# Kernel tuning notes

Hardware: AMD Instinct MI355X
Metric: run time of the kernel (lower is better)

## Reference

```python
import jax, jax.numpy as jnp
import numpy as np
from jax import lax

B, DZ, H, U, T, V = 256, 512, 512, 16, 16, 512  # batch, latent, lstm hidden, segments, steps/segment, vocab


def setup_inputs() -> dict:
    key = jax.random.key(0)
    ks = jax.random.split(key, 32)
    w = lambda k, shape: jax.random.normal(k, shape, jnp.float32) * 0.05
    d = {
        'z': jax.random.normal(ks[0], (B, DZ), jnp.float32),
        'x': jax.random.randint(ks[1], (B, U * T), 0, V),
        # conductor init-state projection: DZ -> 4H
        'Wc': w(ks[2], (4 * H, DZ)), 'bc': jnp.zeros((4 * H,), jnp.float32),
        # conductor 2-layer LSTM (input H, hidden H)
        'cWih0': w(ks[3], (4 * H, H)), 'cWhh0': w(ks[4], (4 * H, H)),
        'cbih0': jnp.zeros((4 * H,), jnp.float32), 'cbhh0': jnp.zeros((4 * H,), jnp.float32),
        'cWih1': w(ks[5], (4 * H, H)), 'cWhh1': w(ks[6], (4 * H, H)),
        'cbih1': jnp.zeros((4 * H,), jnp.float32), 'cbhh1': jnp.zeros((4 * H,), jnp.float32),
        # decoder init-state projection: H -> 4H
        'Wd': w(ks[7], (4 * H, H)), 'bd': jnp.zeros((4 * H,), jnp.float32),
        # decoder 2-layer LSTM (layer0 input 2H, layer1 input H, hidden H)
        'dWih0': w(ks[8], (4 * H, 2 * H)), 'dWhh0': w(ks[9], (4 * H, H)),
        'dbih0': jnp.zeros((4 * H,), jnp.float32), 'dbhh0': jnp.zeros((4 * H,), jnp.float32),
        'dWih1': w(ks[10], (4 * H, H)), 'dWhh1': w(ks[11], (4 * H, H)),
        'dbih1': jnp.zeros((4 * H,), jnp.float32), 'dbhh1': jnp.zeros((4 * H,), jnp.float32),
        # token embedding and output distribution head
        'emb': w(ks[12], (V, H)),
        'Wo': w(ks[13], (V, H)), 'bo': jnp.zeros((V,), jnp.float32),
    }
    return d


def _cell(x, h, c, Wih, Whh, bih, bhh):
    # PyTorch LSTM gate order: i, f, g, o
    g = x @ Wih.T + bih + h @ Whh.T + bhh
    i, f, gg, o = jnp.split(g, 4, axis=-1)
    c = jax.nn.sigmoid(f) * c + jax.nn.sigmoid(i) * jnp.tanh(gg)
    h = jax.nn.sigmoid(o) * jnp.tanh(c)
    return h, c


def _lstm_layer(xp, h0, c0, Whh, bhh):
    # xp: [N, T, 4H] = precomputed x @ Wih.T + bih
    def step(carry, xg):
        h, c = carry
        g = xg + h @ Whh.T + bhh
        i, f, gg, o = jnp.split(g, 4, axis=-1)
        c = jax.nn.sigmoid(f) * c + jax.nn.sigmoid(i) * jnp.tanh(gg)
        h = jax.nn.sigmoid(o) * jnp.tanh(c)
        return (h, c), h
    _, ys = lax.scan(step, (h0, c0), jnp.swapaxes(xp, 0, 1))
    return jnp.swapaxes(ys, 0, 1)  # [N, T, H]


def reference(z, x, Wc, bc, cWih0, cWhh0, cbih0, cbhh0, cWih1, cWhh1, cbih1, cbhh1,
              Wd, bd, dWih0, dWhh0, dbih0, dbhh0, dWih1, dWhh1, dbih1, dbhh1,
              emb, Wo, bo):
    Bz = z.shape[0]
    # --- conductor ---
    ci = jnp.tanh(z @ Wc.T + bc)  # [B, 4H]
    h1, h2, c1, c2 = ci[:, :H], ci[:, H:2 * H], ci[:, 2 * H:3 * H], ci[:, 3 * H:]
    o0 = jnp.zeros((Bz, H), ci.dtype)

    def cstep(carry, _):
        o, h1, c1, h2, c2 = carry
        h1, c1 = _cell(o, h1, c1, cWih0, cWhh0, cbih0, cbhh0)
        h2, c2 = _cell(h1, h2, c2, cWih1, cWhh1, cbih1, cbhh1)
        return (h2, h1, c1, h2, c2), h2

    _, couts = lax.scan(cstep, (o0, h1, c1, h2, c2), None, length=U)
    cond_out = jnp.swapaxes(couts, 0, 1)  # [B, U, H]

    # --- decoder init states ---
    states = jnp.tanh(cond_out @ Wd.T + bd).reshape(Bz * U, 4 * H)
    dh1, dh2, dc1, dc2 = (states[:, :H], states[:, H:2 * H],
                          states[:, 2 * H:3 * H], states[:, 3 * H:])
    h_init = dh1 + dh2  # [BU, H]

    # --- teacher-forced decoder ---
    xt = x.reshape(Bz * U, T)
    e = emb[xt]  # [BU, T, H]
    e = jnp.concatenate([jnp.zeros((Bz * U, 1, H), e.dtype), e[:, :-1]], axis=1)
    inp = jnp.concatenate(
        [e, jnp.broadcast_to(h_init[:, None], (Bz * U, T, H))], axis=-1)  # [BU, T, 2H]

    y0 = _lstm_layer(inp @ dWih0.T + dbih0, dh1, dc1, dWhh0, dbhh0)
    y1 = _lstm_layer(y0 @ dWih1.T + dbih1, dh2, dc2, dWhh1, dbhh1)
    dist = jax.nn.softmax(y1 @ Wo.T + bo, axis=-1)  # [BU, T, V]
    return dist.reshape(Bz, U * T, V)
```

## Files before the change

### kernel.cpp

```cpp
#include <hip/hip_runtime.h>
#include <math.h>

#define AS1 __attribute__((address_space(1)))
#define AS3 __attribute__((address_space(3)))

typedef __attribute__((ext_vector_type(8))) short short8v;
typedef __attribute__((ext_vector_type(16))) float f32x16;

constexpr size_t PA4c = (size_t)4096 * 512;
constexpr size_t PABc = (size_t)256 * 512;

__device__ __forceinline__ float sigmoidf_(float x) { return 1.f / (1.f + expf(-x)); }
__device__ __forceinline__ unsigned int f2bfu(float f) {
    unsigned int u = __float_as_uint(f);
    return (u + 0x7FFF + ((u >> 16) & 1)) >> 16;
}
__device__ __forceinline__ float bf2f(unsigned int s) { return __uint_as_float(s << 16); }
__device__ __forceinline__ unsigned int pack2(float v) {
    unsigned int b0 = f2bfu(v);
    unsigned int b1 = f2bfu(v - bf2f(b0));
    return b0 | (b1 << 16);
}
__device__ __forceinline__ float unpack2(unsigned int p) { return bf2f(p & 0xffffu) + bf2f(p >> 16); }

__device__ __forceinline__ void xswz(int d, int ngx, int ngy, int& bx, int& by) {
    int nwg = ngx * ngy;
    int q = nwg >> 3, r = nwg & 7, xcd = d & 7, pos = d >> 3;
    int logical = (xcd < r ? xcd * (q + 1) : r * (q + 1) + (xcd - r) * q) + pos;
    bx = logical % ngx; by = logical / ngx;
}

__device__ __forceinline__ void xswz_col(int d, int ngx, int ngy, int& bx, int& by) {
    int cpx = ngx >> 3;
    int xcd = d & 7, j = d >> 3;
    bx = xcd * cpx + (j % cpx);
    by = j / cpx;
}

__device__ __forceinline__ size_t offf(int m, int k) {
    return ((size_t)((m >> 5) * 64 + (k >> 3))) * 256 + (size_t)((m & 31) * 8 + (k & 7));
}

template<int N>
__device__ __forceinline__ void wait_vm() {
    asm volatile("s_waitcnt vmcnt(%0) lgkmcnt(0)" :: "n"(N) : "memory");
}

template<int FM, int FN>
__device__ __forceinline__ void gemm_core(
    const short* __restrict__ A1, const short* __restrict__ B1,
    const short* __restrict__ A2, const short* __restrict__ B2,
    int M, int N, int nsteps, int pairSwitch,
    int bx, int by, short* lds, f32x16 (&acc)[FM][FN])
{
    constexpr int ABLK = 4 * FM, BBLK = 2 * FN;
    constexpr int ACH = 2 * ABLK * 2, BCH = 2 * BBLK * 2;
    constexpr int CHT = ACH + BCH;
    constexpr int CPW = CHT / 8;
    constexpr int NBUF = 3;
    constexpr int BUFSH = CHT * 512;
    const int tid = threadIdx.x, lane = tid & 63, wid = tid >> 6;
    const int wm = wid >> 1, wn = wid & 1;
    const int l31 = lane & 31, loct = lane >> 5;
    const int mblk0 = by * ABLK, nblk0 = bx * BBLK;
    const size_t planeA = (size_t)M * 512, planeB = (size_t)N * 512;

    const short* cur[CPW];
    const short* nxt[CPW];
    int ldo[CPW];
    #pragma unroll
    for (int i = 0; i < CPW; ++i) {
        int c = wid * CPW + i;
        ldo[i] = c * 512;
        size_t off;
        const short *b1, *b2;
        if (c < ACH) {
            int plane = c / (ABLK * 2), rem = c % (ABLK * 2), blk = rem >> 1, piece = rem & 1;
            off = (size_t)plane * planeA + (size_t)(mblk0 + blk) * 16384 + piece * 512 + lane * 8;
            b1 = A1; b2 = A2;
        } else {
            int cb = c - ACH;
            int plane = cb / (BBLK * 2), rem = cb % (BBLK * 2), blk = rem >> 1, piece = rem & 1;
            off = (size_t)plane * planeB + (size_t)(nblk0 + blk) * 16384 + piece * 512 + lane * 8;
            b1 = B1; b2 = B2;
        }
        cur[i] = b1 + off;
        nxt[i] = b2 ? (b2 + off) : (b1 + off);
    }

    #pragma unroll
    for (int fm = 0; fm < FM; ++fm)
        #pragma unroll
        for (int fn = 0; fn < FN; ++fn)
            acc[fm][fn] = (f32x16){};

    auto STAGE = [&](int bufIdx) {
        short* db = lds + bufIdx * BUFSH;
        #pragma unroll
        for (int i = 0; i < CPW; ++i) {
            __builtin_amdgcn_global_load_lds((const AS1 unsigned int*)cur[i],
                                             (AS3 unsigned int*)(db + ldo[i]), 16, 0, 0);
            cur[i] += 1024;
        }
    };

    STAGE(0); STAGE(1);
    wait_vm<CPW>();
    __builtin_amdgcn_s_barrier();

    for (int t = 0; t < nsteps; ++t) {
        int s = t + NBUF - 1;
        if (s < nsteps) {
            if (s == pairSwitch) {
                #pragma unroll
                for (int i = 0; i < CPW; ++i) cur[i] = nxt[i];
            }
            STAGE(s % NBUF);
        }
        const short* L = lds + (t % NBUF) * BUFSH;
        #pragma unroll
        for (int ksub = 0; ksub < 2; ++ksub) {
            short8v a[FM][2], b[FN][2];
            #pragma unroll
            for (int p = 0; p < 2; ++p) {
                #pragma unroll
                for (int f = 0; f < FM; ++f)
                    a[f][p] = *(const short8v*)(L + (p * (ABLK * 2) + (wm * FM + f) * 2 + ksub) * 512
                                                  + loct * 256 + l31 * 8);
                #pragma unroll
                for (int f = 0; f < FN; ++f)
                    b[f][p] = *(const short8v*)(L + (ACH + p * (BBLK * 2) + (wn * FN + f) * 2 + ksub) * 512
                                                  + loct * 256 + l31 * 8);
            }
            #pragma unroll
            for (int pp = 0; pp < 3; ++pp) {
                const int pa = (pp == 2) ? 1 : 0, pb = (pp == 1) ? 1 : 0;
                #pragma unroll
                for (int fm = 0; fm < FM; ++fm)
                    #pragma unroll
                    for (int fn = 0; fn < FN; ++fn)
                        acc[fm][fn] = __builtin_amdgcn_mfma_f32_32x32x16_bf16(
                            a[fm][pa], b[fn][pb], acc[fm][fn], 0, 0, 0);
            }
        }
        if (t + 2 < nsteps) wait_vm<CPW>();
        else                wait_vm<0>();
        __builtin_amdgcn_s_barrier();
    }
}

template<int FM, int FN>
__device__ __forceinline__ void epi_f32(f32x16 (&acc)[FM][FN], int bx, int by, int N,
                                        float* __restrict__ Cout, const float* __restrict__ bias, int act)
{
    constexpr int ROWS = 128 * FM, COLS = 64 * FN;
    const int tid = threadIdx.x, lane = tid & 63, wid = tid >> 6;
    const int wm = wid >> 1, wn = wid & 1, l31 = lane & 31, loct = lane >> 5;
    #pragma unroll
    for (int fm = 0; fm < FM; ++fm)
        #pragma unroll
        for (int fn = 0; fn < FN; ++fn) {
            int col = bx * COLS + wn * FN * 32 + fn * 32 + l31;
            int rb  = by * ROWS + wm * FM * 32 + fm * 32 + 4 * loct;
            #pragma unroll
            for (int reg = 0; reg < 16; ++reg) {
                int row = rb + (reg & 3) + 8 * (reg >> 2);
                float xv = acc[fm][fn][reg] + (bias ? bias[row] : 0.f);
                if (act) xv = tanhf(xv);
                Cout[(size_t)row * N + col] = xv;
            }
        }
}

template<int FM, int FN>
__device__ __forceinline__ void epi_pack(f32x16 (&acc)[FM][FN], int bx, int by, int N,
                                         unsigned int* __restrict__ packOut)
{
    constexpr int ROWS = 128 * FM, COLS = 64 * FN;
    const int tid = threadIdx.x, lane = tid & 63, wid = tid >> 6;
    const int wm = wid >> 1, wn = wid & 1, l31 = lane & 31, loct = lane >> 5;
    uint4* P4 = (uint4*)packOut;
    #pragma unroll
    for (int fm = 0; fm < FM; ++fm)
        #pragma unroll
        for (int fn = 0; fn < FN; ++fn) {
            int col = bx * COLS + wn * FN * 32 + fn * 32 + l31;
            int ub = by * (ROWS / 4) + wm * FM * 8 + fm * 8 + loct;
            #pragma unroll
            for (int ug = 0; ug < 4; ++ug) {
                int u = ub + 2 * ug;
                uint4 v;
                v.x = pack2(acc[fm][fn][4 * ug + 0]);
                v.y = pack2(acc[fm][fn][4 * ug + 1]);
                v.z = pack2(acc[fm][fn][4 * ug + 2]);
                v.w = pack2(acc[fm][fn][4 * ug + 3]);
                P4[(size_t)u * N + col] = v;
            }
        }
}

template<int FM, int FN>
__device__ __forceinline__ void epi_gate2(
    f32x16 (&acc)[FM][FN], int bx, int by, int N, short* hl,
    const float* __restrict__ bab,
    const unsigned int* __restrict__ hgP,
    const unsigned int* __restrict__ embT,
    const int* __restrict__ xidx,
    float* __restrict__ cT,
    short* __restrict__ hout, size_t hps,
    short* __restrict__ condp, int ustep)
{
    constexpr int ABLK = 4 * FM, BBLK = 2 * FN;
    constexpr int ROWS = 32 * ABLK, COLS = 32 * BBLK;
    constexpr int CHN = ABLK * BBLK * 256;
    const int tid = threadIdx.x, lane = tid & 63, wid = tid >> 6;
    const int wm = wid >> 1, wn = wid & 1, l31 = lane & 31, loct = lane >> 5;
    #pragma unroll
    for (int fm = 0; fm < FM; ++fm) {
        #pragma unroll
        for (int fn = 0; fn < FN; ++fn) {
            const int col = bx * COLS + wn * FN * 32 + fn * 32 + l31;
            const int ub = by * (ROWS / 4) + wm * FM * 8 + fm * 8 + loct;
            int tok = -1;
            if (xidx) tok = xidx[(size_t)col * 16];
            uint4 hv[4]; uint4 ev[4]; float cv[4]; float4 bv[4];
            #pragma unroll
            for (int ug = 0; ug < 4; ++ug) {
                int u = ub + 2 * ug;
                bv[ug] = *(const float4*)&bab[4 * u];
                cv[ug] = cT[(size_t)u * N + col];
                if (hgP) hv[ug] = ((const uint4*)hgP)[(size_t)u * N + col];
            }
            if (embT && tok >= 0) {
                #pragma unroll
                for (int ug = 0; ug < 4; ++ug) {
                    int u = ub + 2 * ug;
                    ev[ug] = ((const uint4*)embT)[(size_t)u * 512 + tok];
                }
            }
            #pragma unroll
            for (int ug = 0; ug < 4; ++ug) {
                int u = ub + 2 * ug;
                float gi = acc[fm][fn][4 * ug + 0] + bv[ug].x;
                float gf = acc[fm][fn][4 * ug + 1] + bv[ug].y;
                float gg = acc[fm][fn][4 * ug + 2] + bv[ug].z;
                float go = acc[fm][fn][4 * ug + 3] + bv[ug].w;
                if (hgP) {
                    gi += unpack2(hv[ug].x); gf += unpack2(hv[ug].y);
                    gg += unpack2(hv[ug].z); go += unpack2(hv[ug].w);
                }
                if (embT && tok >= 0) {
                    gi += unpack2(ev[ug].x); gf += unpack2(ev[ug].y);
                    gg += unpack2(ev[ug].z); go += unpack2(ev[ug].w);
                }
                float c = sigmoidf_(gf) * cv[ug] + sigmoidf_(gi) * tanhf(gg);
                cT[(size_t)u * N + col] = c;
                float h = sigmoidf_(go) * tanhf(c);
                unsigned int p01 = pack2(h);
                int u_loc = wm * FM * 8 + fm * 8 + loct + 2 * ug;
                int m_loc = wn * FN * 32 + fn * 32 + l31;
                int offl = ((m_loc >> 5) * ABLK + (u_loc >> 3)) * 256 + (m_loc & 31) * 8 + (u_loc & 7);
                hl[offl] = (short)(p01 & 0xffffu);
                hl[CHN + offl] = (short)(p01 >> 16);
                if (condp) {
                    int np = col * 16 + ustep;
                    size_t oc = offf(np, u);
                    condp[oc] = (short)(p01 & 0xffffu);
                    condp[PA4c + oc] = (short)(p01 >> 16);
                }
            }
        }
    }
    __syncthreads();
    constexpr int LB = (ABLK == 8) ? 3 : 2;
    for (int p = 0; p < 2; ++p) {
        for (int jj = tid; jj < CHN / 8; jj += 512) {
            int lc = jj >> 5, m31 = jj & 31;
            int m5 = lc >> LB, u3 = lc & (ABLK - 1);
            size_t gc = (size_t)((bx * BBLK + m5) * 64 + by * ABLK + u3);
            *(short8v*)(hout + p * hps + gc * 256 + m31 * 8) = *(const short8v*)(hl + p * CHN + jj * 8);
        }
    }
}

template<int FM, int FN>
__global__ __launch_bounds__(512, 1) void gemm_packk(
    const short* A1, const short* B1, const short* A2, const short* B2,
    int M, int N, int nsteps, int psw, int colmap, unsigned int* packOut)
{
    __shared__ __align__(16) short lds[3 * (2 * (4 * FM) * 2 + 2 * (2 * FN) * 2) * 512];
    int d = blockIdx.y * gridDim.x + blockIdx.x;
    int bx, by;
    if (colmap) xswz_col(d, gridDim.x, gridDim.y, bx, by);
    else        xswz(d, gridDim.x, gridDim.y, bx, by);
    f32x16 acc[FM][FN];
    gemm_core<FM, FN>(A1, B1, A2, B2, M, N, nsteps, psw, bx, by, lds, acc);
    epi_pack<FM, FN>(acc, bx, by, N, packOut);
}

template<int FM, int FN>
__global__ __launch_bounds__(512, 1) void gemm_split(
    const short* A1, const short* B1, int M, int N, int nsteps, int colmap,
    const float* bias, short* hA, short* hB, size_t ps, float* cA, float* cB)
{
    __shared__ __align__(16) short lds[3 * (2 * (4 * FM) * 2 + 2 * (2 * FN) * 2) * 512];
    int d = blockIdx.y * gridDim.x + blockIdx.x;
    int bx, by;
    if (colmap) xswz_col(d, gridDim.x, gridDim.y, bx, by);
    else        xswz(d, gridDim.x, gridDim.y, bx, by);
    f32x16 acc[FM][FN];
    gemm_core<FM, FN>(A1, B1, nullptr, nullptr, M, N, nsteps, 100, bx, by, lds, acc);
    constexpr int ROWS = 128 * FM, COLS = 64 * FN;
    const int tid = threadIdx.x, lane = tid & 63, wid = tid >> 6;
    const int wm = wid >> 1, wn = wid & 1, l31 = lane & 31, loct = lane >> 5;
    #pragma unroll
    for (int fm = 0; fm < FM; ++fm)
        #pragma unroll
        for (int fn = 0; fn < FN; ++fn) {
            int col = bx * COLS + wn * FN * 32 + fn * 32 + l31;
            int rb  = by * ROWS + wm * FM * 32 + fm * 32 + 4 * loct;
            #pragma unroll
            for (int reg = 0; reg < 16; ++reg) {
                int row = rb + (reg & 3) + 8 * (reg >> 2);
                float xv = tanhf(acc[fm][fn][reg] + bias[row]);
                if (row < 1024) {
                    short* hp = (row < 512) ? hA : hB;
                    size_t o = offf(col, row & 511);
                    unsigned int p01 = pack2(xv);
                    hp[o] = (short)(p01 & 0xffffu);
                    hp[ps + o] = (short)(p01 >> 16);
                } else {
                    float* cp = (row < 1536) ? cA : cB;
                    cp[(size_t)(row & 511) * N + col] = xv;
                }
            }
        }
}

__global__ __launch_bounds__(512, 1) void cond_cell(
    const short* A1, const short* B1, const short* A2, const short* B2,
    int nsteps, int psw,
    const float* bab, float* cT,
    short* hout, short* condp, int ustep)
{
    __shared__ __align__(16) short lds[3 * 24 * 512];
    int d = blockIdx.y * gridDim.x + blockIdx.x;
    int bx, by; xswz(d, gridDim.x, gridDim.y, bx, by);
    f32x16 acc[1][1];
    gemm_core<1, 1>(A1, B1, A2, B2, 2048, 256, nsteps, psw, bx, by, lds, acc);
    epi_gate2<1, 1>(acc, bx, by, 256, lds, bab, nullptr, nullptr, nullptr,
                    cT, hout, PABc, condp, ustep);
}

struct DecArgs {
    const short *dWhh0P, *dWih1P, *dWhh1P, *WoP;
    const float *babd0, *babd1, *bo;
    const unsigned int *hgP, *embT;
    const int* x;
    float *c0T, *c1dT;
    short *h0a, *h0b, *h1da, *h1db;
    float *LgA, *LgB;
    float* out;
    int t;
};

__global__ __launch_bounds__(512, 1) void dec_step(DecArgs A)
{
    __shared__ __align__(16) short lds[3 * 48 * 512];
    const int role = blockIdx.x >> 8;
    const int dd = blockIdx.x & 255;
    const int t = A.t;
    short* h0[2]  = { A.h0a, A.h0b };
    short* h1d[2] = { A.h1da, A.h1db };
    float* Lg[2]  = { A.LgA, A.LgB };

    if (role == 0) {
        if (t <= 15) {
            int pin = t & 1;
            int bx, by; xswz_col(dd, 32, 8, bx, by);
            f32x16 acc[2][2];
            gemm_core<2, 2>(A.dWhh0P, h0[pin], nullptr, nullptr, 2048, 4096, 16, 100, bx, by, lds, acc);
            epi_gate2<2, 2>(acc, bx, by, 4096, lds, A.babd0, A.hgP,
                            t > 0 ? A.embT : nullptr, t > 0 ? A.x + (t - 1) : nullptr,
                            A.c0T, h0[pin ^ 1], PA4c, nullptr, 0);
            __syncthreads();
        }
        if (t >= 2 && t <= 17) {
            int k = t - 2;
            int bx, by; xswz_col(dd, 64, 4, bx, by);
            f32x16 acc1[1][1];
            gemm_core<1, 1>(A.WoP, h1d[(k + 1) & 1], nullptr, nullptr, 512, 4096, 16, 100, bx, by, lds, acc1);
            epi_f32<1, 1>(acc1, bx, by, 4096, Lg[k & 1], nullptr, 0);
        }
    } else {
        if (t >= 1 && t <= 16) {
            int s = t - 1;
            int pin2 = s & 1;
            int bx, by; xswz_col(dd, 32, 8, bx, by);
            f32x16 acc[2][2];
            gemm_core<2, 2>(A.dWih1P, h0[(s + 1) & 1], A.dWhh1P, h1d[pin2],
                            2048, 4096, 32, 16, bx, by, lds, acc);
            epi_gate2<2, 2>(acc, bx, by, 4096, lds, A.babd1, nullptr, nullptr, nullptr,
                            A.c1dT, h1d[pin2 ^ 1], PA4c, nullptr, 0);
            __syncthreads();
        }
        if (t >= 3) {
            int k = t - 3;
            const float* Lsrc = Lg[k & 1];
            float* tile = (float*)lds;
            float* red  = (float*)lds + 16 * 513;
            float* red2 = red + 512;
            const int tid = threadIdx.x;
            const int mj = tid & 15, vs = tid >> 4;
            const int m = dd * 16 + mj;
            float lv[16];
            #pragma unroll
            for (int i = 0; i < 16; ++i) {
                int v = vs * 16 + i;
                lv[i] = Lsrc[(size_t)v * 4096 + m] + A.bo[v];
            }
            float mx = lv[0];
            #pragma unroll
            for (int i = 1; i < 16; ++i) mx = fmaxf(mx, lv[i]);
            red[vs * 16 + mj] = mx;
            __syncthreads();
            for (int o = 16; o >= 1; o >>= 1) {
                if (vs < o) red[vs * 16 + mj] = fmaxf(red[vs * 16 + mj], red[(vs + o) * 16 + mj]);
                __syncthreads();
            }
            mx = red[mj];
            float sum = 0.f;
            #pragma unroll
            for (int i = 0; i < 16; ++i) {
                float e = expf(lv[i] - mx);
                sum += e;
                tile[mj * 513 + vs * 16 + i] = e;
            }
            red2[vs * 16 + mj] = sum;
            __syncthreads();
            for (int o = 16; o >= 1; o >>= 1) {
                if (vs < o) red2[vs * 16 + mj] += red2[(vs + o) * 16 + mj];
                __syncthreads();
            }
            const int r = tid >> 5, c = tid & 31;
            float invr = 1.f / red2[r];
            for (int kk = 0; kk < 16; ++kk) {
                int v = kk * 32 + c;
                A.out[((size_t)(dd * 16 + r) * 16 + k) * 512 + v] = tile[r * 513 + v] * invr;
            }
        }
    }
}

struct PrepEnt { const float* src; const float* src2; void* dst; int ldw, col0, perm, total, op; };
struct PrepArgs { PrepEnt e[18]; int n; };

__global__ void prep_all(PrepArgs pa)
{
    for (int ei = 0; ei < pa.n; ++ei) {
        PrepEnt E = pa.e[ei];
        for (int o = blockIdx.x * 256 + threadIdx.x; o < E.total; o += gridDim.x * 256) {
            if (E.op == 0) {
                int c = o >> 8, w = o & 255, r = w >> 3, jj = w & 7;
                int n = (c >> 6) * 32 + r, k = (c & 63) * 8 + jj;
                int nsrc = E.perm ? ((n >> 2) + 512 * (n & 3)) : n;
                float v = E.src[(size_t)nsrc * E.ldw + E.col0 + k];
                unsigned int b0 = f2bfu(v);
                short* pl = (short*)E.dst;
                pl[o] = (short)b0;
                pl[E.total + o] = (short)f2bfu(v - bf2f(b0));
            } else {
                int src = (o >> 2) + 512 * (o & 3);
                ((float*)E.dst)[o] = E.src[src] + E.src2[src];
            }
        }
    }
}

extern "C" void kernel_launch(void* const* d_in, const int* in_sizes, int n_in,
                              void* d_out, int out_size, void* d_ws, size_t ws_size,
                              hipStream_t stream)
{
    const float* z     = (const float*)d_in[0];
    const int*   x     = (const int*)  d_in[1];
    const float* Wc    = (const float*)d_in[2];
    const float* bc    = (const float*)d_in[3];
    const float* cWih0 = (const float*)d_in[4];
    const float* cWhh0 = (const float*)d_in[5];
    const float* cbih0 = (const float*)d_in[6];
    const float* cbhh0 = (const float*)d_in[7];
    const float* cWih1 = (const float*)d_in[8];
    const float* cWhh1 = (const float*)d_in[9];
    const float* cbih1 = (const float*)d_in[10];
    const float* cbhh1 = (const float*)d_in[11];
    const float* Wd    = (const float*)d_in[12];
    const float* bd    = (const float*)d_in[13];
    const float* dWih0 = (const float*)d_in[14];
    const float* dWhh0 = (const float*)d_in[15];
    const float* dbih0 = (const float*)d_in[16];
    const float* dbhh0 = (const float*)d_in[17];
    const float* dWih1 = (const float*)d_in[18];
    const float* dWhh1 = (const float*)d_in[19];
    const float* dbih1 = (const float*)d_in[20];
    const float* dbhh1 = (const float*)d_in[21];
    const float* emb   = (const float*)d_in[22];
    const float* Wo    = (const float*)d_in[23];
    const float* bo    = (const float*)d_in[24];
    float* out = (float*)d_out;
    (void)in_sizes; (void)n_in; (void)out_size; (void)ws_size;

    char* wsb = (char*)d_ws;
    size_t off = 0;
    auto alloc = [&](size_t bytes) -> void* {
        off = (off + 255) & ~(size_t)255;
        void* p = wsb + off;
        off += bytes;
        return p;
    };
    const size_t PW  = (size_t)2048 * 512;
    const size_t PWo = (size_t)512 * 512;

    short* WcP    = (short*)alloc(2 * PW * 2);
    short* WdP    = (short*)alloc(2 * PW * 2);
    short* dW1P   = (short*)alloc(2 * PW * 2);
    short* dW2P   = (short*)alloc(2 * PW * 2);
    short* cWih0P = (short*)alloc(2 * PW * 2);
    short* cWhh0P = (short*)alloc(2 * PW * 2);
    short* cWih1P = (short*)alloc(2 * PW * 2);
    short* cWhh1P = (short*)alloc(2 * PW * 2);
    short* dWhh0P = (short*)alloc(2 * PW * 2);
    short* dWih1P = (short*)alloc(2 * PW * 2);
    short* dWhh1P = (short*)alloc(2 * PW * 2);
    short* WoP    = (short*)alloc(2 * PWo * 2);
    short* zpl    = (short*)alloc(2 * PABc * 2);
    short* embpl  = (short*)alloc(2 * PWo * 2);
    float* babc0  = (float*)alloc(2048 * 4);
    float* babc1  = (float*)alloc(2048 * 4);
    float* babd0  = (float*)alloc(2048 * 4);
    float* babd1  = (float*)alloc(2048 * 4);
    float* GbufT  = (float*)alloc((size_t)2048 * 4096 * 4);
    unsigned int* hinitgP = (unsigned int*)alloc((size_t)512 * 4096 * 4 * 4);
    unsigned int* embW0P  = (unsigned int*)alloc((size_t)512 * 512 * 4 * 4);
    short* h1pl[2]; short* h2pl[2];
    h1pl[0] = (short*)alloc(2 * PABc * 2);  h1pl[1] = (short*)alloc(2 * PABc * 2);
    h2pl[0] = (short*)alloc(2 * PABc * 2);  h2pl[1] = (short*)alloc(2 * PABc * 2);
    float* c1T = (float*)alloc((size_t)512 * 256 * 4);
    float* c2T = (float*)alloc((size_t)512 * 256 * 4);
    short* condpl = (short*)alloc(2 * PA4c * 2);
    short* h0pl[2];  short* h1dpl[2];
    h0pl[0]  = (short*)alloc(2 * PA4c * 2); h0pl[1]  = (short*)alloc(2 * PA4c * 2);
    h1dpl[0] = (short*)alloc(2 * PA4c * 2); h1dpl[1] = (short*)alloc(2 * PA4c * 2);
    float* c0T  = (float*)alloc((size_t)512 * 4096 * 4);
    float* c1dT = (float*)alloc((size_t)512 * 4096 * 4);

    float* Lg[2] = { GbufT, GbufT + (size_t)512 * 4096 };

    PrepArgs pa; pa.n = 18;
    auto W8 = [](const float* s, void* d, int ldw, int col0, int perm, int total) {
        PrepEnt e; e.src = s; e.src2 = nullptr; e.dst = d; e.ldw = ldw; e.col0 = col0;
        e.perm = perm; e.total = total; e.op = 0; return e;
    };
    auto B8 = [](const float* a, const float* b, void* d) {
        PrepEnt e; e.src = a; e.src2 = b; e.dst = d; e.ldw = 0; e.col0 = 0;
        e.perm = 0; e.total = 2048; e.op = 1; return e;
    };
    pa.e[0]  = W8(Wc,    WcP,    512,  0,   0, 2048 * 512);
    pa.e[1]  = W8(Wd,    WdP,    512,  0,   0, 2048 * 512);
    pa.e[2]  = W8(dWih0, dW1P,   1024, 0,   1, 2048 * 512);
    pa.e[3]  = W8(dWih0, dW2P,   1024, 512, 1, 2048 * 512);
    pa.e[4]  = W8(cWih0, cWih0P, 512,  0,   1, 2048 * 512);
    pa.e[5]  = W8(cWhh0, cWhh0P, 512,  0,   1, 2048 * 512);
    pa.e[6]  = W8(cWih1, cWih1P, 512,  0,   1, 2048 * 512);
    pa.e[7]  = W8(cWhh1, cWhh1P, 512,  0,   1, 2048 * 512);
    pa.e[8]  = W8(dWhh0, dWhh0P, 512,  0,   1, 2048 * 512);
    pa.e[9]  = W8(dWih1, dWih1P, 512,  0,   1, 2048 * 512);
    pa.e[10] = W8(dWhh1, dWhh1P, 512,  0,   1, 2048 * 512);
    pa.e[11] = W8(Wo,    WoP,    512,  0,   0, 512 * 512);
    pa.e[12] = W8(z,     zpl,    512,  0,   0, 256 * 512);
    pa.e[13] = W8(emb,   embpl,  512,  0,   0, 512 * 512);
    pa.e[14] = B8(cbih0, cbhh0, babc0);
    pa.e[15] = B8(cbih1, cbhh1, babc1);
    pa.e[16] = B8(dbih0, dbhh0, babd0);
    pa.e[17] = B8(dbih1, dbhh1, babd1);
    prep_all<<<dim3(1024), dim3(256), 0, stream>>>(pa);

    gemm_split<2, 2><<<dim3(2, 8), dim3(512), 0, stream>>>(
        WcP, zpl, 2048, 256, 16, 0, bc, h1pl[0], h2pl[0], PABc, c1T, c2T);

    gemm_packk<2, 2><<<dim3(4, 8), dim3(512), 0, stream>>>(
        dW1P, embpl, nullptr, nullptr, 2048, 512, 16, 100, 0, embW0P);

    for (int u = 0; u < 16; ++u) {
        int pin = u & 1;
        if (u == 0)
            cond_cell<<<dim3(4, 16), dim3(512), 0, stream>>>(
                cWhh0P, h1pl[0], nullptr, nullptr, 16, 100,
                babc0, c1T, h1pl[1], nullptr, 0);
        else
            cond_cell<<<dim3(4, 16), dim3(512), 0, stream>>>(
                cWih0P, h2pl[pin], cWhh0P, h1pl[pin], 32, 16,
                babc0, c1T, h1pl[pin ^ 1], nullptr, 0);
        cond_cell<<<dim3(4, 16), dim3(512), 0, stream>>>(
            cWih1P, h1pl[pin ^ 1], cWhh1P, h2pl[pin], 32, 16,
            babc1, c2T, h2pl[pin ^ 1], condpl, u);
    }

    gemm_split<2, 2><<<dim3(32, 8), dim3(512), 0, stream>>>(
        WdP, condpl, 2048, 4096, 16, 1, bd, h0pl[0], h1dpl[0], PA4c, c0T, c1dT);

    gemm_packk<2, 2><<<dim3(32, 8), dim3(512), 0, stream>>>(
        dW2P, h0pl[0], dW2P, h1dpl[0], 2048, 4096, 32, 16, 1, hinitgP);

    for (int t = 0; t <= 18; ++t) {
        DecArgs A;
        A.dWhh0P = dWhh0P; A.dWih1P = dWih1P; A.dWhh1P = dWhh1P; A.WoP = WoP;
        A.babd0 = babd0; A.babd1 = babd1; A.bo = bo;
        A.hgP = hinitgP; A.embT = embW0P; A.x = x;
        A.c0T = c0T; A.c1dT = c1dT;
        A.h0a = h0pl[0]; A.h0b = h0pl[1]; A.h1da = h1dpl[0]; A.h1db = h1dpl[1];
        A.LgA = Lg[0]; A.LgB = Lg[1];
        A.out = out; A.t = t;
        dec_step<<<dim3(512), dim3(512), 0, stream>>>(A);
    }
}
```

Measured before the change: 2.423 ms.

## Load weight tiles straight to registers and deepen LDS pipeline for activations

Adds a new GEMM core for the decoder LSTM steps. Each wave loads its A (weight) fragments directly from global memory into registers, double-buffered across k-steps, so only the B (hidden-state) tiles are staged through LDS, using a 6-deep ring of global_load_lds copies. Waits now cover only vector-memory counters, and MFMA blocks are wrapped in s_setprio. The aim is to cut LDS traffic and space and to hide more load latency, at the cost of extra VGPR pressure from the register-held A tiles and a smaller LDS allocation that the epilogue must still fit into.

Result: no change. 2.458 ms (+1.4%).

```diff
diff --git a/kernel.cpp b/kernel.cpp
--- a/kernel.cpp
+++ b/kernel.cpp
@@ -44,6 +44,10 @@
 template<int N>
 __device__ __forceinline__ void wait_vm() {
     asm volatile("s_waitcnt vmcnt(%0) lgkmcnt(0)" :: "n"(N) : "memory");
+}
+template<int N>
+__device__ __forceinline__ void wait_vm_only() {
+    asm volatile("s_waitcnt vmcnt(%0)" :: "n"(N) : "memory");
 }
 
 template<int FM, int FN>
@@ -145,6 +149,105 @@
         }
         if (t + 2 < nsteps) wait_vm<CPW>();
         else                wait_vm<0>();
+        __builtin_amdgcn_s_barrier();
+    }
+}
+
+template<int FM, int FN>
+__device__ __forceinline__ void gemm_coreAR(
+    const short* __restrict__ A1, const short* __restrict__ B1,
+    const short* __restrict__ A2, const short* __restrict__ B2,
+    int M, int N, int nsteps, int psw,
+    int bx, int by, short* lds, f32x16 (&acc)[FM][FN])
+{
+    constexpr int ABLK = 4 * FM, BBLK = 2 * FN;
+    constexpr int BCH = 2 * BBLK * 2;
+    constexpr int CPW = BCH / 8;
+    constexpr int NBUF = 6;
+    constexpr int BUFSH = BCH * 512;
+    const int tid = threadIdx.x, lane = tid & 63, wid = tid >> 6;
+    const int wm = wid >> 1, wn = wid & 1;
+    const int l31 = lane & 31, loct = lane >> 5;
+    const int mblk0 = by * ABLK, nblk0 = bx * BBLK;
+    const size_t planeA = (size_t)M * 512, planeB = (size_t)N * 512;
+
+    #pragma unroll
+    for (int fm = 0; fm < FM; ++fm)
+        #pragma unroll
+        for (int fn = 0; fn < FN; ++fn)
+            acc[fm][fn] = (f32x16){};
+
+    auto LOADA = [&](int t, short8v (&dst)[FM][2][2]) {
+        const short* As; size_t tb;
+        if (t >= psw) { As = A2; tb = (size_t)(t - psw) * 1024; }
+        else          { As = A1; tb = (size_t)t * 1024; }
+        #pragma unroll
+        for (int f = 0; f < FM; ++f)
+            #pragma unroll
+            for (int p = 0; p < 2; ++p)
+                #pragma unroll
+                for (int ks = 0; ks < 2; ++ks)
+                    dst[f][p][ks] = *(const short8v*)(As + (size_t)p * planeA
+                        + (size_t)(mblk0 + wm * FM + f) * 16384 + tb + ks * 512 + lane * 8);
+    };
+    auto STAGEB = [&](int s) {
+        const short* Bs; size_t tb;
+        if (s >= psw) { Bs = B2; tb = (size_t)(s - psw) * 1024; }
+        else          { Bs = B1; tb = (size_t)s * 1024; }
+        short* db = lds + (s % NBUF) * BUFSH;
+        #pragma unroll
+        for (int i = 0; i < CPW; ++i) {
+            int c = wid * CPW + i;
+            int p = c / (BBLK * 2), rem = c % (BBLK * 2), blk = rem >> 1, piece = rem & 1;
+            __builtin_amdgcn_global_load_lds(
+                (const AS1 unsigned int*)(Bs + (size_t)p * planeB
+                    + (size_t)(nblk0 + blk) * 16384 + tb + piece * 512 + lane * 8),
+                (AS3 unsigned int*)(db + c * 512), 16, 0, 0);
+        }
+    };
+    auto COMPUTE = [&](int t, short8v (&areg)[FM][2][2]) {
+        const short* L = lds + (t % NBUF) * BUFSH;
+        #pragma unroll
+        for (int ks = 0; ks < 2; ++ks) {
+            short8v b[FN][2];
+            #pragma unroll
+            for (int p = 0; p < 2; ++p)
+                #pragma unroll
+                for (int f = 0; f < FN; ++f)
+                    b[f][p] = *(const short8v*)(L + (p * (BBLK * 2) + (wn * FN + f) * 2 + ks) * 512
+                                                  + loct * 256 + l31 * 8);
+            __builtin_amdgcn_s_setprio(1);
+            #pragma unroll
+            for (int pp = 0; pp < 3; ++pp) {
+                const int pa = (pp == 2) ? 1 : 0, pb = (pp == 1) ? 1 : 0;
+                #pragma unroll
+                for (int fm = 0; fm < FM; ++fm)
+                    #pragma unroll
+                    for (int fn = 0; fn < FN; ++fn)
+                        acc[fm][fn] = __builtin_amdgcn_mfma_f32_32x32x16_bf16(
+                            areg[fm][pa][ks], b[fn][pb], acc[fm][fn], 0, 0, 0);
+            }
+            __builtin_amdgcn_s_setprio(0);
+        }
+    };
+
+    short8v aA[FM][2][2], aB[FM][2][2];
+    LOADA(0, aA);
+    #pragma unroll
+    for (int i = 0; i < NBUF - 1; ++i) STAGEB(i);
+    wait_vm_only<(NBUF - 2) * CPW>();
+    __builtin_amdgcn_s_barrier();
+
+    for (int t = 0; t < nsteps; t += 2) {
+        if (t + 1 < nsteps) LOADA(t + 1, aB);
+        if (t + 5 < nsteps) STAGEB(t + 5);
+        COMPUTE(t, aA);
+        wait_vm_only<CPW>();
+        __builtin_amdgcn_s_barrier();
+        if (t + 2 < nsteps) LOADA(t + 2, aA);
+        if (t + 6 < nsteps) STAGEB(t + 6);
+        COMPUTE(t + 1, aB);
+        wait_vm_only<CPW>();
         __builtin_amdgcn_s_barrier();
     }
 }
@@ -366,7 +469,7 @@
 
 __global__ __launch_bounds__(512, 1) void dec_step(DecArgs A)
 {
-    __shared__ __align__(16) short lds[3 * 48 * 512];
+    __shared__ __align__(16) short lds[6 * 16 * 512];
     const int role = blockIdx.x >> 8;
     const int dd = blockIdx.x & 255;
     const int t = A.t;
@@ -379,7 +482,8 @@
             int pin = t & 1;
             int bx, by; xswz_col(dd, 32, 8, bx, by);
             f32x16 acc[2][2];
-            gemm_core<2, 2>(A.dWhh0P, h0[pin], nullptr, nullptr, 2048, 4096, 16, 100, bx, by, lds, acc);
+            gemm_coreAR<2, 2>(A.dWhh0P, h0[pin], A.dWhh0P, h0[pin],
+                              2048, 4096, 16, 100, bx, by, lds, acc);
             epi_gate2<2, 2>(acc, bx, by, 4096, lds, A.babd0, A.hgP,
                             t > 0 ? A.embT : nullptr, t > 0 ? A.x + (t - 1) : nullptr,
                             A.c0T, h0[pin ^ 1], PA4c, nullptr, 0);
@@ -398,8 +502,8 @@
             int pin2 = s & 1;
             int bx, by; xswz_col(dd, 32, 8, bx, by);
             f32x16 acc[2][2];
-            gemm_core<2, 2>(A.dWih1P, h0[(s + 1) & 1], A.dWhh1P, h1d[pin2],
-                            2048, 4096, 32, 16, bx, by, lds, acc);
+            gemm_coreAR<2, 2>(A.dWih1P, h0[(s + 1) & 1], A.dWhh1P, h1d[pin2],
+                              2048, 4096, 32, 16, bx, by, lds, acc);
             epi_gate2<2, 2>(acc, bx, by, 4096, lds, A.babd1, nullptr, nullptr, nullptr,
                             A.c1dT, h1d[pin2 ^ 1], PA4c, nullptr, 0);
             __syncthreads();
```
